# Kernel tuning notes

Measured on AMD Instinct MI355X. Metric: run time of the kernel, lower is better.

The kernel has to match this reference:

```python
import jax, jax.numpy as jnp
import numpy as np

NEG = -9.0e15

def gat_layer(X, adj_mask, W, Wb, a1, a2, ab):
    # X: [N, Fin]; W: [Fin, Fout]; a1,a2: [Fout]; ab: scalar
    h = X @ W + Wb                                   # [N, Fout]
    # a([h_i || h_j]) = h_i@a1 + h_j@a2 + ab  (decomposition of concat+linear)
    e = jax.nn.leaky_relu((h @ a1)[:, None] + (h @ a2)[None, :] + ab,
                          negative_slope=0.2)        # [N, N]
    e = jnp.where(adj_mask, e, NEG)
    attn = jax.nn.softmax(e, axis=1)                 # [N, N]
    return jax.nn.elu(attn @ h)                      # [N, Fout]

def setup_inputs() -> dict:
    key = jax.random.key(0)
    ks = jax.random.split(key, 12)
    N, Fin, Fh, H, Fout = 4096, 512, 128, 4, 64
    X = jax.random.normal(ks[0], (N, Fin), dtype=jnp.float32)
    adjacency_matrix = jax.random.randint(ks[1], (N, N), 0, 2, dtype=jnp.int32)
    s_in = 1.0 / np.sqrt(Fin)
    s_a = 1.0 / np.sqrt(2 * Fh)
    W_h  = jax.random.uniform(ks[2], (H, Fin, Fh), jnp.float32, -s_in, s_in)
    b_h  = jax.random.uniform(ks[3], (H, Fh), jnp.float32, -s_in, s_in)
    a1_h = jax.random.uniform(ks[4], (H, Fh), jnp.float32, -s_a, s_a)
    a2_h = jax.random.uniform(ks[5], (H, Fh), jnp.float32, -s_a, s_a)
    ab_h = jax.random.uniform(ks[6], (H,), jnp.float32, -s_a, s_a)
    Fcat = H * Fh
    s_c = 1.0 / np.sqrt(Fcat)
    s_ao = 1.0 / np.sqrt(2 * Fout)
    W_o  = jax.random.uniform(ks[7], (Fcat, Fout), jnp.float32, -s_c, s_c)
    b_o  = jax.random.uniform(ks[8], (Fout,), jnp.float32, -s_c, s_c)
    a1_o = jax.random.uniform(ks[9], (Fout,), jnp.float32, -s_ao, s_ao)
    a2_o = jax.random.uniform(ks[10], (Fout,), jnp.float32, -s_ao, s_ao)
    ab_o = jax.random.uniform(ks[11], (), jnp.float32, -s_ao, s_ao)
    return {"X": X, "adjacency_matrix": adjacency_matrix,
            "W_h": W_h, "b_h": b_h, "a1_h": a1_h, "a2_h": a2_h, "ab_h": ab_h,
            "W_o": W_o, "b_o": b_o, "a1_o": a1_o, "a2_o": a2_o, "ab_o": ab_o}

def reference(X, adjacency_matrix, W_h, b_h, a1_h, a2_h, ab_h,
              W_o, b_o, a1_o, a2_o, ab_o):
    adj_mask = adjacency_matrix > 0
    # per-head attention layers, vmapped over heads
    heads = jax.vmap(gat_layer, in_axes=(None, None, 0, 0, 0, 0, 0))(
        X, adj_mask, W_h, b_h, a1_h, a2_h, ab_h)      # [H, N, Fh]
    H, N, Fh = heads.shape
    x = jnp.transpose(heads, (1, 0, 2)).reshape(N, H * Fh)  # concat along features
    x = gat_layer(x, adj_mask, W_o, b_o, a1_o, a2_o, ab_o)  # [N, Fout]
    return jax.nn.log_softmax(x, axis=1)
```

## Files before the change

kernel.cpp:

```cpp
#include <hip/hip_runtime.h>
#include <math.h>

#define NN 4096
#define LOG2E 1.44269504088896340736f

using f32x4  = __attribute__((ext_vector_type(4))) float;
using bf16x4 = __attribute__((ext_vector_type(4))) __bf16;
using bf16x8 = __attribute__((ext_vector_type(8))) __bf16;

#if __has_builtin(__builtin_amdgcn_exp2f)
#define EXP2(x) __builtin_amdgcn_exp2f(x)
#else
#define EXP2(x) __expf((x) * 0.6931471805599453f)
#endif

#define WAITVM4_BARRIER asm volatile("s_waitcnt vmcnt(4)\ns_barrier" ::: "memory")
#define WAITVM0_BARRIER asm volatile("s_waitcnt vmcnt(0)\ns_barrier" ::: "memory")

template<int FH>
__device__ __forceinline__ void stage_tile(const __bf16* __restrict__ hgp,
                                           __bf16* dst, int tid) {
#pragma unroll
    for (int it = 0; it < FH / 32; it++) {
        int c = tid + it * 256;
        int f = c >> 3, sl = c & 7;
        int g = sl ^ (f & 7);
        __builtin_amdgcn_global_load_lds(
            (const __attribute__((address_space(1))) void*)(hgp + (size_t)f * NN + g * 8),
            (__attribute__((address_space(3))) void*)(dst + (size_t)c * 8), 16, 0, 0);
    }
}

__device__ __forceinline__ void stage_g(const __bf16* __restrict__ base, int ldk,
                                        __bf16* dst, int tid) {
#pragma unroll
    for (int it = 0; it < 2; it++) {
        int c = tid + it * 256;
        int f = c >> 3, sl = c & 7;
        int g = sl ^ (f & 7);
        __builtin_amdgcn_global_load_lds(
            (const __attribute__((address_space(1))) void*)(base + (size_t)f * ldk + g * 8),
            (__attribute__((address_space(3))) void*)(dst + (size_t)c * 8), 16, 0, 0);
    }
}

__global__ void prep_kernel(const int* __restrict__ adj, unsigned long long* __restrict__ bits,
                            const float* __restrict__ W_h, const float* __restrict__ b_h,
                            const float* __restrict__ W_o,
                            __bf16* __restrict__ Bt1, float* __restrict__ biasp,
                            __bf16* __restrict__ Bt2,
                            const float* __restrict__ X, __bf16* __restrict__ Xb,
                            float* __restrict__ zeros) {
    const int b = blockIdx.x, t = threadIdx.x;
    if (b < 1024) {
        int idx = b * 256 + t;
        {
            int n = idx >> 9, k = idx & 511;
            int h = n >> 7, f = n & 127;
            Bt1[idx] = (__bf16)W_h[(size_t)h * 512 * 128 + k * 128 + f];
        }
        if (idx < 64 * 512) {
            int n = idx >> 9, k = idx & 511;
            Bt2[idx] = (__bf16)W_o[k * 64 + n];
        }
        if (idx < 512) biasp[idx] = b_h[idx];
        if (idx < (10 * NN) / 4)
            *(f32x4*)(zeros + (size_t)idx * 4) = (f32x4){0.f, 0.f, 0.f, 0.f};
    } else if (b < 3072) {
        int i = (b - 1024) * 256 + t;
        f32x4 v = *(const f32x4*)(X + (size_t)i * 4);
        bf16x4 o;
#pragma unroll
        for (int q = 0; q < 4; q++) o[q] = (__bf16)v[q];
        *(bf16x4*)(Xb + (size_t)i * 4) = o;
    } else {
        int wave = (b - 3072) * 4 + (t >> 6);
        int lane = t & 63;
        int g0 = wave * 16;
        for (int it = 0; it < 16; it++) {
            int gw = g0 + it;
            int v = adj[(size_t)gw * 64 + lane];
            unsigned long long m = __ballot(v > 0);
            if (lane == 0) bits[gw] = m;
        }
    }
}

template<int FUSEA>
__global__ __launch_bounds__(256) void gemm_fused_kernel(
    const __bf16* __restrict__ A, const __bf16* __restrict__ Bt,
    const float* __restrict__ bias,
    const float* __restrict__ a1, const float* __restrict__ a2,
    __bf16* __restrict__ Ht, float* __restrict__ s1, float* __restrict__ s2,
    const __bf16* __restrict__ accp, const float* __restrict__ lgin,
    int M, int N, int K)
{
    constexpr int NB = FUSEA ? 2 : 3;
    __shared__ __attribute__((aligned(16))) __bf16 As[NB][64 * 64];
    __shared__ __attribute__((aligned(16))) __bf16 Bs[NB][64 * 64];
    __shared__ float sinv[4][64];
    const int tid = threadIdx.x, w = tid >> 6, l = tid & 63, o = l >> 4, rl = l & 15;
    const int bm = blockIdx.y * 64, bn = blockIdx.x * 64;
    f32x4 acc[4] = {};
    const int KB = K / 64;

    auto stageA_fused = [&](int kb, __bf16* dst) {
#pragma unroll
        for (int it = 0; it < 2; it++) {
            int c = tid + it * 256;
            int f = c >> 3, sl = c & 7;
            int row = bm + f;
            int col = kb * 64 + sl * 8;
            float inv = sinv[kb >> 1][f];
            float vs[8] = {0.f, 0.f, 0.f, 0.f, 0.f, 0.f, 0.f, 0.f};
#pragma unroll
            for (int js = 0; js < 4; js++) {
                bf16x8 t = *(const bf16x8*)(accp + ((size_t)js * NN + row) * 512 + col);
#pragma unroll
                for (int q = 0; q < 8; q++) vs[q] += (float)t[q];
            }
            bf16x8 ob;
#pragma unroll
            for (int q = 0; q < 8; q++) {
                float x = vs[q] * inv;
                x = x > 0.f ? x : __expf(x) - 1.f;
                ob[q] = (__bf16)x;
            }
            *(bf16x8*)(dst + ((size_t)f * 8 + (sl ^ (f & 7))) * 8) = ob;
        }
    };

    if constexpr (FUSEA) {
        {
            int h = tid >> 6, r = tid & 63;
            float ls = 0.f;
#pragma unroll
            for (int js = 0; js < 4; js++) ls += lgin[((size_t)(h * 4 + js)) * NN + bm + r];
            sinv[h][r] = ls > 0.f ? 1.f / ls : 0.f;
        }
        __syncthreads();
        stageA_fused(0, &As[0][0]);
        stage_g(Bt + (size_t)bn * K, K, &Bs[0][0], tid);
        for (int kb = 0; kb < KB; kb++) {
            int b = kb & 1;
            __syncthreads();
            if (kb + 1 < KB) {
                stageA_fused(kb + 1, &As[b ^ 1][0]);
                stage_g(Bt + (size_t)bn * K + (kb + 1) * 64, K, &Bs[b ^ 1][0], tid);
            }
#pragma unroll
            for (int kt = 0; kt < 2; kt++) {
                int ra = w * 16 + rl;
                int cg = kt * 4 + o;
                bf16x8 af = *(const bf16x8*)(&As[b][(ra * 8 + (cg ^ (ra & 7))) * 8]);
#pragma unroll
                for (int nt = 0; nt < 4; nt++) {
                    int rb = nt * 16 + rl;
                    bf16x8 bfr = *(const bf16x8*)(&Bs[b][(rb * 8 + (cg ^ (rb & 7))) * 8]);
                    acc[nt] = __builtin_amdgcn_mfma_f32_16x16x32_bf16(af, bfr, acc[nt], 0, 0, 0);
                }
            }
        }
    } else {
        stage_g(A + (size_t)bm * K, K, &As[0][0], tid);
        stage_g(Bt + (size_t)bn * K, K, &Bs[0][0], tid);
        stage_g(A + (size_t)bm * K + 64, K, &As[1][0], tid);
        stage_g(Bt + (size_t)bn * K + 64, K, &Bs[1][0], tid);
        int b = 0;
        for (int kb = 0; kb < KB; kb++) {
            if (kb + 1 < KB) { WAITVM4_BARRIER; }
            else             { WAITVM0_BARRIER; }
#pragma unroll
            for (int kt = 0; kt < 2; kt++) {
                int ra = w * 16 + rl;
                int cg = kt * 4 + o;
                bf16x8 af = *(const bf16x8*)(&As[b][(ra * 8 + (cg ^ (ra & 7))) * 8]);
#pragma unroll
                for (int nt = 0; nt < 4; nt++) {
                    int rb = nt * 16 + rl;
                    bf16x8 bfr = *(const bf16x8*)(&Bs[b][(rb * 8 + (cg ^ (rb & 7))) * 8]);
                    acc[nt] = __builtin_amdgcn_mfma_f32_16x16x32_bf16(af, bfr, acc[nt], 0, 0, 0);
                }
            }
            if (kb + 2 < KB) {
                int b2 = b + 2; if (b2 >= 3) b2 -= 3;
                stage_g(A + (size_t)bm * K + (kb + 2) * 64, K, &As[b2][0], tid);
                stage_g(Bt + (size_t)bn * K + (kb + 2) * 64, K, &Bs[b2][0], tid);
            }
            if (++b == 3) b = 0;
        }
    }
    const int head = bn >> 7;
    const int row_base = bm + w * 16 + o * 4;
    float p1[4] = {0.f, 0.f, 0.f, 0.f}, p2[4] = {0.f, 0.f, 0.f, 0.f};
#pragma unroll
    for (int nt = 0; nt < 4; nt++) {
        int col = bn + nt * 16 + rl;
        float bv = bias[col];
        float a1v = a1[col] * LOG2E, a2v = a2[col] * LOG2E;
        bf16x4 hv;
#pragma unroll
        for (int r4 = 0; r4 < 4; r4++) {
            float h = acc[nt][r4] + bv;
            hv[r4] = (__bf16)h;
            p1[r4] += h * a1v;
            p2[r4] += h * a2v;
        }
        *(bf16x4*)(Ht + (size_t)col * M + row_base) = hv;
    }
#pragma unroll
    for (int r4 = 0; r4 < 4; r4++)
#pragma unroll
        for (int off = 1; off < 16; off <<= 1) {
            p1[r4] += __shfl_xor(p1[r4], off, 64);
            p2[r4] += __shfl_xor(p2[r4], off, 64);
        }
    if (rl == 0)
#pragma unroll
        for (int r4 = 0; r4 < 4; r4++) {
            atomicAdd(&s1[(size_t)head * M + row_base + r4], p1[r4]);
            atomicAdd(&s2[(size_t)head * M + row_base + r4], p2[r4]);
        }
}

template<int FH, int JSPLIT>
__global__ __launch_bounds__(256, 4) void attn_kernel(
    const __bf16* __restrict__ Htg,
    const unsigned long long* __restrict__ adj_bits,
    const float* __restrict__ s1_all, const float* __restrict__ s2_all,
    const float* __restrict__ ab_all,
    __bf16* __restrict__ accp,
    float* __restrict__ lg,
    int ldo)
{
    constexpr int NJT = NN / 64 / JSPLIT;
    constexpr int NTL = FH / 16;
    const int head = blockIdx.y;
    const int js   = blockIdx.z;
    const int row0 = blockIdx.x * 64;
    const int jt0  = js * NJT;
    const int tid = threadIdx.x;
    const int w = tid >> 6, l = tid & 63, o = l >> 4, rl = l & 15;
    const int myrow = row0 + w * 16 + rl;

    __shared__ __attribute__((aligned(16))) __bf16 hbuf[2][FH * 64];
    __shared__ __attribute__((aligned(16))) float el1[NJT * 64];
    __shared__ __attribute__((aligned(16))) float el2[NJT * 64];

    const float* s2 = s2_all + (size_t)head * NN;
    const __bf16* hg = Htg + (size_t)head * FH * NN;
    const float s1r = s1_all[(size_t)head * NN + myrow] + ab_all[head] * LOG2E;
    const float F1 = EXP2(s1r);
    const float F2 = EXP2(0.2f * s1r);
    float lacc = 0.f;
    f32x4 acc[NTL] = {};

    unsigned long long aw;
    auto PLOAD = [&](int jt) { aw = adj_bits[(size_t)myrow * 64 + jt]; };
    auto PMATH = [&](int jl, bf16x8& f0, bf16x8& f1) {
        float ps = 0.f;
#pragma unroll
        for (int kt = 0; kt < 2; kt++) {
            unsigned int mb = (unsigned int)(aw >> ((kt * 4 + o) * 8)) & 0xFFu;
            int eb = jl * 64 + kt * 32 + o * 8;
            f32x4 e1a = *(const f32x4*)(&el1[eb]);
            f32x4 e1b = *(const f32x4*)(&el1[eb + 4]);
            f32x4 e2a = *(const f32x4*)(&el2[eb]);
            f32x4 e2b = *(const f32x4*)(&el2[eb + 4]);
#pragma unroll
            for (int q = 0; q < 8; q++) {
                float e1 = (q < 4) ? e1a[q] : e1b[q - 4];
                float e2 = (q < 4) ? e2a[q] : e2b[q - 4];
                float p = fmaxf(F1 * e1, F2 * e2);
                p = ((mb >> q) & 1u) ? p : 0.f;
                if (kt == 0) f0[q] = (__bf16)p; else f1[q] = (__bf16)p;
                ps += p;
            }
        }
        lacc += ps;
    };

    stage_tile<FH>(hg + (size_t)jt0 * 64, &hbuf[0][0], tid);
    for (int i = tid; i < NJT * 64; i += 256) {
        float s = s2[jt0 * 64 + i];
        el1[i] = EXP2(s);
        el2[i] = EXP2(0.2f * s);
    }
    PLOAD(jt0);
    __syncthreads();
    bf16x8 fc0, fc1, fn0, fn1;
    PMATH(0, fc0, fc1);
    if (NJT > 1) PLOAD(jt0 + 1);

    for (int jl = 0; jl < NJT; jl++) {
        const int b = jl & 1;
        const int jt = jt0 + jl;
        __syncthreads();
        if (jl + 1 < NJT)
            stage_tile<FH>(hg + (size_t)(jt + 1) * 64, &hbuf[b ^ 1][0], tid);
        if (jl + 1 < NJT) PMATH(jl + 1, fn0, fn1);
        if (jl + 2 < NJT) PLOAD(jt + 2);
        __builtin_amdgcn_s_setprio(1);
#pragma unroll
        for (int ntl = 0; ntl < NTL; ntl++) {
            int f = ntl * 16 + rl;
            int s0 = o ^ (rl & 7);
            int s1 = (4 + o) ^ (rl & 7);
            bf16x8 b0 = *(const bf16x8*)(&hbuf[b][(f * 8 + s0) * 8]);
            bf16x8 b1 = *(const bf16x8*)(&hbuf[b][(f * 8 + s1) * 8]);
            acc[ntl] = __builtin_amdgcn_mfma_f32_16x16x32_bf16(fc0, b0, acc[ntl], 0, 0, 0);
            acc[ntl] = __builtin_amdgcn_mfma_f32_16x16x32_bf16(fc1, b1, acc[ntl], 0, 0, 0);
        }
        __builtin_amdgcn_s_setprio(0);
        if (jl + 1 < NJT) { fc0 = fn0; fc1 = fn1; }
    }
    lacc += __shfl_xor(lacc, 16, 64);
    lacc += __shfl_xor(lacc, 32, 64);
    if (l < 16) lg[((size_t)head * JSPLIT + js) * NN + row0 + w * 16 + l] = lacc;
#pragma unroll
    for (int ntl = 0; ntl < NTL; ntl++)
#pragma unroll
        for (int r4 = 0; r4 < 4; r4++) {
            int grow = row0 + w * 16 + o * 4 + r4;
            int gcol = head * FH + ntl * 16 + rl;
            accp[((size_t)js * NN + grow) * ldo + gcol] = (__bf16)acc[ntl][r4];
        }
}

__global__ void combine2_kernel(const __bf16* __restrict__ accp, const float* __restrict__ lg,
                                float* __restrict__ out) {
    int row = (blockIdx.x * 256 + threadIdx.x) >> 6;
    int lane = threadIdx.x & 63;
    if (row >= NN) return;
    float lsum = 0.f, v = 0.f;
#pragma unroll
    for (int js = 0; js < 16; js++) {
        lsum += lg[(size_t)js * NN + row];
        v += (float)accp[((size_t)js * NN + row) * 64 + lane];
    }
    float inv = lsum > 0.f ? 1.f / lsum : 0.f;
    v *= inv;
    v = v > 0.f ? v : __expf(v) - 1.f;
    float m = v;
#pragma unroll
    for (int off = 1; off < 64; off <<= 1) m = fmaxf(m, __shfl_xor(m, off, 64));
    float ex = __expf(v - m);
    float s = ex;
#pragma unroll
    for (int off = 1; off < 64; off <<= 1) s += __shfl_xor(s, off, 64);
    out[(size_t)row * 64 + lane] = v - m - __logf(s);
}

extern "C" void kernel_launch(void* const* d_in, const int* in_sizes, int n_in,
                              void* d_out, int out_size, void* d_ws, size_t ws_size,
                              hipStream_t stream) {
    const float* X    = (const float*)d_in[0];
    const int*   adj  = (const int*)d_in[1];
    const float* W_h  = (const float*)d_in[2];
    const float* b_h  = (const float*)d_in[3];
    const float* a1_h = (const float*)d_in[4];
    const float* a2_h = (const float*)d_in[5];
    const float* ab_h = (const float*)d_in[6];
    const float* W_o  = (const float*)d_in[7];
    const float* b_o  = (const float*)d_in[8];
    const float* a1_o = (const float*)d_in[9];
    const float* a2_o = (const float*)d_in[10];
    const float* ab_o = (const float*)d_in[11];
    float* out = (float*)d_out;

    char* ws = (char*)d_ws;
    auto alloc = [&](size_t bytes) {
        char* p = ws; ws += (bytes + 255) & ~(size_t)255; return p;
    };
    unsigned long long* adj_bits = (unsigned long long*)alloc((size_t)NN * 64 * 8);
    __bf16* Bt1    = (__bf16*)alloc((size_t)512 * 512 * 2);
    float*  biasp  = (float*)alloc(512 * 4);
    __bf16* Bt2    = (__bf16*)alloc((size_t)64 * 512 * 2);
    __bf16* Xb     = (__bf16*)alloc((size_t)NN * 512 * 2);
    float*  s1h    = (float*)alloc((size_t)4 * NN * 4);
    float*  s2h    = (float*)alloc((size_t)4 * NN * 4);
    float*  s1o    = (float*)alloc((size_t)NN * 4);
    float*  s2o    = (float*)alloc((size_t)NN * 4);
    __bf16* Htg    = (__bf16*)alloc((size_t)512 * NN * 2);
    __bf16* accp1  = (__bf16*)alloc((size_t)4 * NN * 512 * 2);
    float*  lg1    = (float*)alloc((size_t)16 * NN * 4);
    __bf16* Ht2    = (__bf16*)alloc((size_t)64 * NN * 2);
    __bf16* accp2  = (__bf16*)alloc((size_t)16 * NN * 64 * 2);
    float*  lg2    = (float*)alloc((size_t)16 * NN * 4);

    prep_kernel<<<7168, 256, 0, stream>>>(adj, adj_bits, W_h, b_h, W_o,
                                          Bt1, biasp, Bt2, X, Xb, s1h);
    gemm_fused_kernel<0><<<dim3(8, 64), 256, 0, stream>>>(
        Xb, Bt1, biasp, a1_h, a2_h, Htg, s1h, s2h, nullptr, nullptr, NN, 512, 512);
    attn_kernel<128, 4><<<dim3(NN / 64, 4, 4), 256, 0, stream>>>(
        Htg, adj_bits, s1h, s2h, ab_h, accp1, lg1, 512);
    gemm_fused_kernel<1><<<dim3(1, 64), 256, 0, stream>>>(
        nullptr, Bt2, b_o, a1_o, a2_o, Ht2, s1o, s2o, accp1, lg1, NN, 64, 512);
    attn_kernel<64, 16><<<dim3(NN / 64, 1, 16), 256, 0, stream>>>(
        Ht2, adj_bits, s1o, s2o, ab_o, accp2, lg2, 64);
    combine2_kernel<<<(NN * 64) / 256, 256, 0, stream>>>(accp2, lg2, out);
}
```

Measured before the change: 199.1 us.

## Use 8-wave attention blocks with finer column split and overlap workspace buffers

The first-layer attention kernel now runs 512-thread blocks covering 128 rows, so each staged H tile is reused by twice as many rows. The column range is split into 8 chunks instead of 4, giving more parallel blocks. The second GEMM therefore sums 8 partial accumulators instead of 4, which doubles partial-sum traffic. The workspace is rearranged so Xb, accp1, accp2 and lg2 alias one region, reducing memory footprint. The risks are more global reads in the fused reduction and possible hazards from the aliased buffers.

```diff
diff --git a/kernel.cpp b/kernel.cpp
--- a/kernel.cpp
+++ b/kernel.cpp
@@ -17,12 +17,12 @@
 #define WAITVM4_BARRIER asm volatile("s_waitcnt vmcnt(4)\ns_barrier" ::: "memory")
 #define WAITVM0_BARRIER asm volatile("s_waitcnt vmcnt(0)\ns_barrier" ::: "memory")
 
-template<int FH>
+template<int FH, int THREADS>
 __device__ __forceinline__ void stage_tile(const __bf16* __restrict__ hgp,
                                            __bf16* dst, int tid) {
 #pragma unroll
-    for (int it = 0; it < FH / 32; it++) {
-        int c = tid + it * 256;
+    for (int it = 0; it < FH * 64 / 8 / THREADS; it++) {
+        int c = tid + it * THREADS;
         int f = c >> 3, sl = c & 7;
         int g = sl ^ (f & 7);
         __builtin_amdgcn_global_load_lds(
@@ -96,6 +96,7 @@
     int M, int N, int K)
 {
     constexpr int NB = FUSEA ? 2 : 3;
+    constexpr int JS1 = 8;
     __shared__ __attribute__((aligned(16))) __bf16 As[NB][64 * 64];
     __shared__ __attribute__((aligned(16))) __bf16 Bs[NB][64 * 64];
     __shared__ float sinv[4][64];
@@ -114,7 +115,7 @@
             float inv = sinv[kb >> 1][f];
             float vs[8] = {0.f, 0.f, 0.f, 0.f, 0.f, 0.f, 0.f, 0.f};
 #pragma unroll
-            for (int js = 0; js < 4; js++) {
+            for (int js = 0; js < JS1; js++) {
                 bf16x8 t = *(const bf16x8*)(accp + ((size_t)js * NN + row) * 512 + col);
 #pragma unroll
                 for (int q = 0; q < 8; q++) vs[q] += (float)t[q];
@@ -135,7 +136,8 @@
             int h = tid >> 6, r = tid & 63;
             float ls = 0.f;
 #pragma unroll
-            for (int js = 0; js < 4; js++) ls += lgin[((size_t)(h * 4 + js)) * NN + bm + r];
+            for (int js = 0; js < JS1; js++)
+                ls += lgin[((size_t)(h * JS1 + js)) * NN + bm + r];
             sinv[h][r] = ls > 0.f ? 1.f / ls : 0.f;
         }
         __syncthreads();
@@ -223,8 +225,8 @@
         }
 }
 
-template<int FH, int JSPLIT>
-__global__ __launch_bounds__(256, 4) void attn_kernel(
+template<int FH, int JSPLIT, int NWAVES>
+__global__ __launch_bounds__(NWAVES * 64, NWAVES) void attn_kernel(
     const __bf16* __restrict__ Htg,
     const unsigned long long* __restrict__ adj_bits,
     const float* __restrict__ s1_all, const float* __restrict__ s2_all,
@@ -235,9 +237,10 @@
 {
     constexpr int NJT = NN / 64 / JSPLIT;
     constexpr int NTL = FH / 16;
+    constexpr int THREADS = NWAVES * 64;
     const int head = blockIdx.y;
     const int js   = blockIdx.z;
-    const int row0 = blockIdx.x * 64;
+    const int row0 = blockIdx.x * (NWAVES * 16);
     const int jt0  = js * NJT;
     const int tid = threadIdx.x;
     const int w = tid >> 6, l = tid & 63, o = l >> 4, rl = l & 15;
@@ -280,8 +283,8 @@
         lacc += ps;
     };
 
-    stage_tile<FH>(hg + (size_t)jt0 * 64, &hbuf[0][0], tid);
-    for (int i = tid; i < NJT * 64; i += 256) {
+    stage_tile<FH, THREADS>(hg + (size_t)jt0 * 64, &hbuf[0][0], tid);
+    for (int i = tid; i < NJT * 64; i += THREADS) {
         float s = s2[jt0 * 64 + i];
         el1[i] = EXP2(s);
         el2[i] = EXP2(0.2f * s);
@@ -297,7 +300,7 @@
         const int jt = jt0 + jl;
         __syncthreads();
         if (jl + 1 < NJT)
-            stage_tile<FH>(hg + (size_t)(jt + 1) * 64, &hbuf[b ^ 1][0], tid);
+            stage_tile<FH, THREADS>(hg + (size_t)(jt + 1) * 64, &hbuf[b ^ 1][0], tid);
         if (jl + 1 < NJT) PMATH(jl + 1, fn0, fn1);
         if (jl + 2 < NJT) PLOAD(jt + 2);
         __builtin_amdgcn_s_setprio(1);
@@ -373,30 +376,31 @@
         char* p = ws; ws += (bytes + 255) & ~(size_t)255; return p;
     };
     unsigned long long* adj_bits = (unsigned long long*)alloc((size_t)NN * 64 * 8);
-    __bf16* Bt1    = (__bf16*)alloc((size_t)512 * 512 * 2);
-    float*  biasp  = (float*)alloc(512 * 4);
     __bf16* Bt2    = (__bf16*)alloc((size_t)64 * 512 * 2);
-    __bf16* Xb     = (__bf16*)alloc((size_t)NN * 512 * 2);
     float*  s1h    = (float*)alloc((size_t)4 * NN * 4);
     float*  s2h    = (float*)alloc((size_t)4 * NN * 4);
     float*  s1o    = (float*)alloc((size_t)NN * 4);
     float*  s2o    = (float*)alloc((size_t)NN * 4);
+    float*  lg1    = (float*)alloc((size_t)32 * NN * 4);
+    __bf16* Ht2    = (__bf16*)alloc((size_t)64 * NN * 2);
+    float*  biasp  = (float*)alloc(512 * 4);
     __bf16* Htg    = (__bf16*)alloc((size_t)512 * NN * 2);
-    __bf16* accp1  = (__bf16*)alloc((size_t)4 * NN * 512 * 2);
-    float*  lg1    = (float*)alloc((size_t)16 * NN * 4);
-    __bf16* Ht2    = (__bf16*)alloc((size_t)64 * NN * 2);
-    __bf16* accp2  = (__bf16*)alloc((size_t)16 * NN * 64 * 2);
-    float*  lg2    = (float*)alloc((size_t)16 * NN * 4);
+    __bf16* Bt1    = (__bf16*)alloc((size_t)512 * 512 * 2);
+    char*   ovl    = alloc((size_t)8 * NN * 512 * 2);
+    __bf16* Xb     = (__bf16*)ovl;
+    __bf16* accp1  = (__bf16*)ovl;
+    __bf16* accp2  = (__bf16*)ovl;
+    float*  lg2    = (float*)(ovl + (size_t)16 * NN * 64 * 2);
 
     prep_kernel<<<7168, 256, 0, stream>>>(adj, adj_bits, W_h, b_h, W_o,
                                           Bt1, biasp, Bt2, X, Xb, s1h);
     gemm_fused_kernel<0><<<dim3(8, 64), 256, 0, stream>>>(
         Xb, Bt1, biasp, a1_h, a2_h, Htg, s1h, s2h, nullptr, nullptr, NN, 512, 512);
-    attn_kernel<128, 4><<<dim3(NN / 64, 4, 4), 256, 0, stream>>>(
+    attn_kernel<128, 8, 8><<<dim3(NN / 128, 4, 8), 512, 0, stream>>>(
         Htg, adj_bits, s1h, s2h, ab_h, accp1, lg1, 512);
     gemm_fused_kernel<1><<<dim3(1, 64), 256, 0, stream>>>(
         nullptr, Bt2, b_o, a1_o, a2_o, Ht2, s1o, s2o, accp1, lg1, NN, 64, 512);
-    attn_kernel<64, 16><<<dim3(NN / 64, 1, 16), 256, 0, stream>>>(
+    attn_kernel<64, 16, 4><<<dim3(NN / 64, 1, 16), 256, 0, stream>>>(
         Ht2, adj_bits, s1o, s2o, ab_o, accp2, lg2, 64);
     combine2_kernel<<<(NN * 64) / 256, 256, 0, stream>>>(accp2, lg2, out);
 }
```

Result: slower. 330.6 us (+66.0%).
